# Performance work log

Measured on AMD Instinct MI355X. Metric: run time of the kernel, lower is better.

The kernel has to match this reference:

```python
import math
import jax, jax.numpy as jnp
import numpy as np

S = 2048
HIDDEN = 5120
H = 16              # num_local_heads (128 global heads / TP=8)
NOPE, ROPE, V = 128, 64, 128
QK = NOPE + ROPE    # 192 (module pads to 256; zero-pad is a mathematical no-op)
QLORA, KVLORA = 1536, 512
EPS = 1e-6
BASE, FACTOR = 10000.0, 40.0
BETA_FAST, BETA_SLOW = 32.0, 1.0
ORIG_MAX = 4096
MSCALE = MSCALE_ALL = 0.707


def _yarn_get_mscale(scale, mscale):
    if scale <= 1:
        return 1.0
    return 0.1 * mscale * math.log(scale) + 1.0


SCALING = QK ** -0.5 * _yarn_get_mscale(FACTOR, MSCALE_ALL) ** 2
COS_SIN_MSCALE = _yarn_get_mscale(FACTOR, MSCALE) / _yarn_get_mscale(FACTOR, MSCALE_ALL)


def _yarn_inv_freq():
    half = ROPE // 2
    i = np.arange(half, dtype=np.float64)
    pos_freqs = BASE ** (2.0 * i / ROPE)
    inv_extra = 1.0 / pos_freqs
    inv_interp = 1.0 / (FACTOR * pos_freqs)

    def corr_dim(n_rot):
        return ROPE * math.log(ORIG_MAX / (n_rot * 2 * math.pi)) / (2 * math.log(BASE))

    low = max(math.floor(corr_dim(BETA_FAST)), 0)
    high = min(math.ceil(corr_dim(BETA_SLOW)), ROPE - 1)
    ramp = np.clip((i - low) / max(high - low, 1e-3), 0.0, 1.0)
    inv_freq_mask = 1.0 - ramp  # 1 -> extrapolation, 0 -> interpolation
    inv_freq = inv_interp * (1.0 - inv_freq_mask) + inv_extra * inv_freq_mask
    return jnp.asarray(inv_freq, dtype=jnp.float32)


INV_FREQ = _yarn_inv_freq()  # [ROPE/2]


def _apply_rope(x, cos, sin):
    # non-neox (interleaved pairs): x [S, heads, ROPE], cos/sin [S, ROPE/2]
    x1 = x[..., 0::2]
    x2 = x[..., 1::2]
    c = cos[:, None, :]
    s = sin[:, None, :]
    o1 = x1 * c - x2 * s
    o2 = x2 * c + x1 * s
    return jnp.stack([o1, o2], axis=-1).reshape(x.shape)


def _rms_norm(x, w):
    var = jnp.mean(x.astype(jnp.float32) ** 2, axis=-1, keepdims=True)
    return (x.astype(jnp.float32) * jax.lax.rsqrt(var + EPS)).astype(x.dtype) * w


def setup_inputs() -> dict:
    key = jax.random.key(0)
    ks = jax.random.split(key, 8)
    sd = 0.02
    return {
        'positions': jnp.arange(S, dtype=jnp.int64 if jax.config.jax_enable_x64 else jnp.int32),
        'hidden_states': jax.random.normal(ks[0], (S, HIDDEN), jnp.float32),
        'w_q_a': jax.random.normal(ks[1], (HIDDEN, QLORA), jnp.float32) * sd,
        'q_a_ln_w': jnp.ones((QLORA,), jnp.float32),
        'w_q_b': jax.random.normal(ks[2], (QLORA, H * QK), jnp.float32) * sd,
        'w_kv_a': jax.random.normal(ks[3], (HIDDEN, KVLORA + ROPE), jnp.float32) * sd,
        'kv_a_ln_w': jnp.ones((KVLORA,), jnp.float32),
        'w_kv_b': jax.random.normal(ks[4], (KVLORA, H * (NOPE + V)), jnp.float32) * sd,
        'w_o': jax.random.normal(ks[5], (H * V, HIDDEN), jnp.float32) * sd,
    }


def reference(positions, hidden_states, w_q_a, q_a_ln_w, w_q_b, w_kv_a, kv_a_ln_w, w_kv_b, w_o):
    # Q low-rank path: q_a_proj -> RMSNorm -> q_b_proj
    q = hidden_states @ w_q_a                       # [S, QLORA]
    q = _rms_norm(q, q_a_ln_w)
    q = (q @ w_q_b).reshape(S, H, QK)               # [S, H, 192]
    q_nope, q_pe = q[..., :NOPE], q[..., NOPE:]

    # KV latent path: shared MQA latent + decoupled rope key
    latent = hidden_states @ w_kv_a                 # [S, KVLORA+ROPE]
    kv_a = _rms_norm(latent[:, :KVLORA], kv_a_ln_w)
    k_pe = latent[:, None, KVLORA:]                 # [S, 1, ROPE]
    kv = (kv_a @ w_kv_b).reshape(S, H, NOPE + V)
    k_nope, v = kv[..., :NOPE], kv[..., NOPE:]

    # partial (decoupled) yarn RoPE on the 64-dim rope slice
    freqs = positions.astype(jnp.float32)[:, None] * INV_FREQ[None, :]
    cos = jnp.cos(freqs) * COS_SIN_MSCALE
    sin = jnp.sin(freqs) * COS_SIN_MSCALE
    q_pe = _apply_rope(q_pe, cos, sin)
    k_pe = _apply_rope(k_pe, cos, sin)

    qf = jnp.concatenate([q_nope, q_pe], axis=-1)   # [S, H, 192]
    kf = jnp.concatenate([k_nope, jnp.broadcast_to(k_pe, (S, H, ROPE))], axis=-1)

    # causal paged-attention prefill; zero-padding head dims to 256 is a no-op
    scores = jnp.einsum('qhd,khd->hqk', qf, kf) * SCALING  # [H, S, S]
    causal = jnp.tril(jnp.ones((S, S), dtype=bool))
    scores = jnp.where(causal[None], scores, -jnp.inf)
    probs = jax.nn.softmax(scores, axis=-1)
    attn = jnp.einsum('hqk,khd->qhd', probs, v).reshape(S, H * V)
    return attn @ w_o                               # [S, HIDDEN]
```

## Files before the change

kernel.cpp:

```cpp
#include <hip/hip_runtime.h>
#include <math.h>

typedef unsigned short u16;
typedef unsigned int u32;
typedef __attribute__((ext_vector_type(4))) float f32x4;
typedef __attribute__((ext_vector_type(8))) unsigned short u16x8;
typedef __attribute__((ext_vector_type(4))) unsigned short u16x4;
typedef __attribute__((ext_vector_type(8))) __bf16 bf16x8;

#define DEV __device__ __forceinline__

constexpr int S = 2048;
constexpr int HIDDEN = 5120;
constexpr int H = 16;
constexpr int NOPE = 128, ROPE_D = 64, VD = 128;
constexpr int QKD = NOPE + ROPE_D;
constexpr int QLORA = 1536, KVLORA = 512;
constexpr int KVA_N = KVLORA + ROPE_D;
constexpr float SCALING = 0.11472134f;

DEV u16 f2b(float f) {
  u32 u = __builtin_bit_cast(u32, f);
  u32 r = u + 0x7FFFu + ((u >> 16) & 1u);
  return (u16)(r >> 16);
}
DEV float b2f(u16 h) { return __builtin_bit_cast(float, (u32)h << 16); }

DEV void store_out(float* p, float v) { *p = v; }
DEV void store_out(u16* p, float v) { *p = f2b(v); }

DEV void gload_lds16(const u16* g, u16* l) {
  auto* gp = (const __attribute__((address_space(1))) u16*)g;
  auto* lp = (__attribute__((address_space(3))) u16*)l;
  __builtin_amdgcn_global_load_lds(gp, lp, 16, 0, 0);
}

#define SWZ(row, col) ((col) ^ (((row) & 7) << 3))

DEV void transpose_tile(const float* __restrict__ in, u16* __restrict__ out,
                        int R, int C, int c0, int r0, int tid, float (*tl)[33]) {
  int tx = tid & 31, ty = tid >> 5;
  for (int r = ty; r < 32; r += 8)
    tl[r][tx] = in[(size_t)(r0 + r) * C + c0 + tx];
  __syncthreads();
  for (int r = ty; r < 32; r += 8)
    out[(size_t)(c0 + r) * R + r0 + tx] = f2b(tl[tx][r]);
}

__global__ __launch_bounds__(256) void k_prep(const float* __restrict__ hidden, u16* __restrict__ hs_bf,
                                              const float* __restrict__ w_q_a, u16* __restrict__ bt_qa,
                                              const float* __restrict__ w_kv_a, u16* __restrict__ bt_kva,
                                              const float* __restrict__ w_q_b, u16* __restrict__ bt_qb,
                                              const float* __restrict__ w_kv_b, u16* __restrict__ bt_kvb,
                                              float* __restrict__ cs, float* __restrict__ sn) {
  __shared__ float tl[32][33];
  int b = blockIdx.x, tid = threadIdx.x;
  if (b < 10240) {
    int i = (b * 256 + tid) * 4;
    f32x4 v = *reinterpret_cast<const f32x4*>(hidden + i);
    u16x4 o;
    o[0] = f2b(v[0]); o[1] = f2b(v[1]); o[2] = f2b(v[2]); o[3] = f2b(v[3]);
    *reinterpret_cast<u16x4*>(hs_bf + i) = o;
    return;
  }
  b -= 10240;
  if (b < 7680) {
    transpose_tile(w_q_a, bt_qa, HIDDEN, QLORA, (b % 48) * 32, (b / 48) * 32, tid, tl);
    return;
  }
  b -= 7680;
  if (b < 2880) {
    transpose_tile(w_kv_a, bt_kva, HIDDEN, KVA_N, (b % 18) * 32, (b / 18) * 32, tid, tl);
    return;
  }
  b -= 2880;
  if (b < 4608) {
    transpose_tile(w_q_b, bt_qb, QLORA, H * QKD, (b % 96) * 32, (b / 96) * 32, tid, tl);
    return;
  }
  b -= 4608;
  if (b < 2048) {
    transpose_tile(w_kv_b, bt_kvb, KVLORA, H * 256, (b % 128) * 32, (b / 128) * 32, tid, tl);
    return;
  }
  b -= 2048;
  int idx = b * 256 + tid;
  int s = idx >> 5, j = idx & 31;
  double pf = pow(10000.0, (double)j / 32.0);
  double inv_extra = 1.0 / pf;
  double inv_interp = 1.0 / (40.0 * pf);
  double twopi = 6.283185307179586476925286766559;
  double lnb2 = 2.0 * log(10000.0);
  double lowd = floor(64.0 * log(4096.0 / (32.0 * twopi)) / lnb2);
  if (lowd < 0.0) lowd = 0.0;
  double highd = ceil(64.0 * log(4096.0 / twopi) / lnb2);
  if (highd > 63.0) highd = 63.0;
  double denom = highd - lowd;
  if (denom < 0.001) denom = 0.001;
  double ramp = ((double)j - lowd) / denom;
  ramp = ramp < 0.0 ? 0.0 : (ramp > 1.0 ? 1.0 : ramp);
  float invf = (float)(inv_interp * ramp + inv_extra * (1.0 - ramp));
  float fr = (float)s * invf;
  cs[idx] = cosf(fr);
  sn[idx] = sinf(fr);
}

template <typename OutT>
DEV void gemm_body(u16* Al, u16* Bl, const u16* __restrict__ A,
                   const u16* __restrict__ BT, OutT* __restrict__ C,
                   int N, int Kstride, int Klen, int mbase, int nbase) {
  const int tid = threadIdx.x;
  const int lane = tid & 63, wave = tid >> 6;
  const int wr = wave >> 1, wc = wave & 1;
  const int lr = lane & 15, lk = lane >> 4;
  const int srow = wave * 32 + (lane >> 2);
  const int skoff = (((lane & 3) ^ ((lane >> 3) & 3))) * 8;
  const int swlk8 = (lk ^ ((lr >> 1) & 3)) * 8;
  const u16* aptr = A + (size_t)(mbase + srow) * Kstride + skoff;
  const u16* bptr = BT + (size_t)(nbase + srow) * Kstride + skoff;
  u16* alw = Al + wave * (32 * 32);
  u16* blw = Bl + wave * (32 * 32);

  auto STAGE = [&](int b, int kk) {
    gload_lds16(aptr + kk, alw + b * 4096);
    gload_lds16(aptr + (size_t)16 * Kstride + kk, alw + b * 4096 + 16 * 32);
    gload_lds16(bptr + kk, blw + b * 4096);
    gload_lds16(bptr + (size_t)16 * Kstride + kk, blw + b * 4096 + 16 * 32);
  };

  f32x4 acc[4][4];
#pragma unroll
  for (int mf = 0; mf < 4; ++mf)
#pragma unroll
    for (int nf = 0; nf < 4; ++nf) acc[mf][nf] = {0.f, 0.f, 0.f, 0.f};

  const int nt = Klen >> 5;
  STAGE(0, 0);
  STAGE(1, 32);
  for (int t = 0; t < nt; ++t) {
    const int cur = t & 1;
    if (t + 1 < nt)
      asm volatile("s_waitcnt vmcnt(4)" ::: "memory");
    else
      asm volatile("s_waitcnt vmcnt(0)" ::: "memory");
    __builtin_amdgcn_s_barrier();
    const u16* Ac = Al + cur * 4096;
    const u16* Bc = Bl + cur * 4096;
    bf16x8 af[4], bfr[4];
#pragma unroll
    for (int mf = 0; mf < 4; ++mf)
      af[mf] = *reinterpret_cast<const bf16x8*>(Ac + (wr * 64 + mf * 16 + lr) * 32 + swlk8);
#pragma unroll
    for (int nf = 0; nf < 4; ++nf)
      bfr[nf] = *reinterpret_cast<const bf16x8*>(Bc + (wc * 64 + nf * 16 + lr) * 32 + swlk8);
#pragma unroll
    for (int mf = 0; mf < 4; ++mf)
#pragma unroll
      for (int nf = 0; nf < 4; ++nf)
        acc[mf][nf] = __builtin_amdgcn_mfma_f32_16x16x32_bf16(af[mf], bfr[nf], acc[mf][nf], 0, 0, 0);
    __builtin_amdgcn_s_barrier();
    if (t + 2 < nt) STAGE(cur, (t + 2) * 32);
  }

#pragma unroll
  for (int mf = 0; mf < 4; ++mf)
#pragma unroll
    for (int nf = 0; nf < 4; ++nf) {
      int col = nbase + wc * 64 + nf * 16 + lr;
      if (col < N) {
#pragma unroll
        for (int r = 0; r < 4; ++r) {
          int row = mbase + wr * 64 + mf * 16 + lk * 4 + r;
          store_out(&C[(size_t)row * N + col], acc[mf][nf][r]);
        }
      }
    }
}

__global__ __launch_bounds__(256) void k_gemm_out(const u16* __restrict__ A,
                                                  const u16* __restrict__ BT,
                                                  float* __restrict__ C) {
  __shared__ u16 Al[2 * 128 * 32];
  __shared__ u16 Bl[2 * 128 * 32];
  int id = blockIdx.x;
  int row = id & 15, col = id >> 4;
  gemm_body(Al, Bl, A, BT, C, HIDDEN, H * VD, H * VD, row * 128, col * 128);
}

__global__ __launch_bounds__(256) void k_gemm_up(const u16* __restrict__ Aq, const u16* __restrict__ Bq,
                                                 u16* __restrict__ Cq,
                                                 const u16* __restrict__ Akv, const u16* __restrict__ Bkv,
                                                 u16* __restrict__ Ckv) {
  __shared__ u16 Al[2 * 128 * 32];
  __shared__ u16 Bl[2 * 128 * 32];
  int id = blockIdx.x;
  int row = id & 15, col = id >> 4;
  if (col < 24)
    gemm_body(Al, Bl, Aq, Bq, Cq, H * QKD, QLORA, QLORA, row * 128, col * 128);
  else
    gemm_body(Al, Bl, Akv, Bkv, Ckv, H * 256, KVLORA, KVLORA, row * 128, (col - 24) * 128);
}

__global__ __launch_bounds__(256) void k_gemm_dp(const u16* __restrict__ A,
                                                 const u16* __restrict__ Bq,
                                                 const u16* __restrict__ Bkv,
                                                 float* __restrict__ q0, float* __restrict__ q1,
                                                 float* __restrict__ l0, float* __restrict__ l1) {
  __shared__ u16 Al[2 * 128 * 32];
  __shared__ u16 Bl[2 * 128 * 32];
  constexpr int KH = HIDDEN / 2;
  int id = blockIdx.x;
  int split = id >= 272;
  int u = id - split * 272;
  int row = u & 15, colt = u >> 4;
  const u16* As = A + split * KH;
  if (colt < 12) {
    gemm_body(Al, Bl, As, Bq + split * KH, split ? q1 : q0, QLORA, HIDDEN, KH,
              row * 128, colt * 128);
  } else {
    gemm_body(Al, Bl, As, Bkv + split * KH, split ? l1 : l0, KVA_N, HIDDEN, KH,
              row * 128, (colt - 12) * 128);
  }
}

DEV void rmsnorm2_row(const float* __restrict__ x0, const float* __restrict__ x1,
                      const float* __restrict__ w, u16* __restrict__ y,
                      int ncols, int instride, int row, int tid, float* red) {
  const float* xr0 = x0 + (size_t)row * instride;
  const float* xr1 = x1 + (size_t)row * instride;
  float ss = 0.f;
  for (int i = tid * 4; i < ncols; i += 1024) {
    f32x4 a = *reinterpret_cast<const f32x4*>(xr0 + i);
    f32x4 b = *reinterpret_cast<const f32x4*>(xr1 + i);
    f32x4 v = a + b;
    ss += v[0] * v[0] + v[1] * v[1] + v[2] * v[2] + v[3] * v[3];
  }
  for (int off = 32; off > 0; off >>= 1) ss += __shfl_down(ss, off);
  if ((tid & 63) == 0) red[tid >> 6] = ss;
  __syncthreads();
  ss = red[0] + red[1] + red[2] + red[3];
  float sc = rsqrtf(ss / (float)ncols + 1e-6f);
  u16* yr = y + (size_t)row * ncols;
  for (int i = tid * 4; i < ncols; i += 1024) {
    f32x4 a = *reinterpret_cast<const f32x4*>(xr0 + i);
    f32x4 b = *reinterpret_cast<const f32x4*>(xr1 + i);
    f32x4 v = a + b;
    u16x4 o;
    o[0] = f2b(v[0] * sc * w[i]);
    o[1] = f2b(v[1] * sc * w[i + 1]);
    o[2] = f2b(v[2] * sc * w[i + 2]);
    o[3] = f2b(v[3] * sc * w[i + 3]);
    *reinterpret_cast<u16x4*>(yr + i) = o;
  }
}

__global__ __launch_bounds__(256) void k_mid(const float* __restrict__ q0, const float* __restrict__ q1,
                                             const float* __restrict__ qw, u16* __restrict__ q_ln,
                                             const float* __restrict__ l0, const float* __restrict__ l1,
                                             const float* __restrict__ kw, u16* __restrict__ kv_ln,
                                             const float* __restrict__ w_o, u16* __restrict__ bt_o) {
  __shared__ float red[4];
  __shared__ float tl[32][33];
  int b = blockIdx.x, tid = threadIdx.x;
  if (b < 2048) {
    rmsnorm2_row(q0, q1, qw, q_ln, QLORA, QLORA, b, tid, red);
    return;
  }
  if (b < 4096) {
    rmsnorm2_row(l0, l1, kw, kv_ln, KVLORA, KVA_N, b - 2048, tid, red);
    return;
  }
  int u = b - 4096;
  transpose_tile(w_o, bt_o, H * VD, HIDDEN, (u % 160) * 32, (u / 160) * 32, tid, tl);
}

__global__ __launch_bounds__(256) void k_build(const u16* __restrict__ qn,
                                               const u16* __restrict__ kv,
                                               const float* __restrict__ lat0,
                                               const float* __restrict__ lat1,
                                               const float* __restrict__ cs,
                                               const float* __restrict__ sn,
                                               u16* __restrict__ qf, u16* __restrict__ kf,
                                               u16* __restrict__ vt) {
  __shared__ u16 tv[32][33];
  int b = blockIdx.x, tid = threadIdx.x;
  if (b < 2048) {
    int s = b;
    for (int idx = tid; idx < H * NOPE; idx += 256) {
      int h = idx >> 7, dd = idx & 127;
      qf[((size_t)h * S + s) * QKD + dd] = qn[(size_t)s * (H * QKD) + h * QKD + dd];
      kf[((size_t)h * S + s) * QKD + dd] = kv[(size_t)s * (H * 256) + h * 256 + dd];
    }
    for (int idx = tid; idx < H * 32; idx += 256) {
      int h = idx >> 5, j = idx & 31;
      float c = cs[s * 32 + j], si = sn[s * 32 + j];
      float x1 = b2f(qn[(size_t)s * (H * QKD) + h * QKD + NOPE + 2 * j]);
      float x2 = b2f(qn[(size_t)s * (H * QKD) + h * QKD + NOPE + 2 * j + 1]);
      qf[((size_t)h * S + s) * QKD + NOPE + 2 * j] = f2b(x1 * c - x2 * si);
      qf[((size_t)h * S + s) * QKD + NOPE + 2 * j + 1] = f2b(x2 * c + x1 * si);
      float k1 = lat0[(size_t)s * KVA_N + KVLORA + 2 * j] + lat1[(size_t)s * KVA_N + KVLORA + 2 * j];
      float k2 = lat0[(size_t)s * KVA_N + KVLORA + 2 * j + 1] + lat1[(size_t)s * KVA_N + KVLORA + 2 * j + 1];
      kf[((size_t)h * S + s) * QKD + NOPE + 2 * j] = f2b(k1 * c - k2 * si);
      kf[((size_t)h * S + s) * QKD + NOPE + 2 * j + 1] = f2b(k2 * c + k1 * si);
    }
    return;
  }
  int bb = b - 2048;
  int s0 = (bb & 63) * 32, d0 = ((bb >> 6) & 3) * 32, h = bb >> 8;
  int tx = tid & 31, ty = tid >> 5;
  for (int r = ty; r < 32; r += 8)
    tv[r][tx] = kv[(size_t)(s0 + r) * (H * 256) + h * 256 + NOPE + d0 + tx];
  __syncthreads();
  for (int r = ty; r < 32; r += 8)
    vt[((size_t)h * VD + d0 + r) * S + s0 + tx] = tv[tx][r];
}

__global__ __launch_bounds__(256) void k_attn(const u16* __restrict__ qf,
                                              const u16* __restrict__ kf,
                                              const u16* __restrict__ vt,
                                              u16* __restrict__ attn) {
  const int bidx = blockIdx.x;
  const int j = bidx & 31;
  const int h = bidx >> 5;
  const int qt = (h < 8) ? j : 31 - j;
  const int qbase = qt * 64;
  const int tid = threadIdx.x, wave = tid >> 6, lane = tid & 63;
  const int lr = lane & 15, lk = lane >> 4;
  __shared__ u16 Kl[64][192];
  __shared__ u16 Vl[128][64];
  __shared__ u16 Pl[4][16][64];

  int krow_[6], kofs_[6], vrow_[4], vofs_[4];
#pragma unroll
  for (int i = 0; i < 6; ++i) { int c = tid + i * 256; krow_[i] = c / 24; kofs_[i] = (c % 24) * 8; }
#pragma unroll
  for (int i = 0; i < 4; ++i) { int c = tid + i * 256; vrow_[i] = c >> 3; vofs_[i] = (c & 7) * 8; }
  const u16* kfh = kf + (size_t)h * S * QKD;
  const u16* vth = vt + (size_t)h * VD * S;

  bf16x8 qfrag[6];
  const u16* qrow = qf + ((size_t)h * S + qbase + wave * 16 + lr) * QKD;
#pragma unroll
  for (int d = 0; d < 6; ++d)
    qfrag[d] = *reinterpret_cast<const bf16x8*>(qrow + d * 32 + lk * 8);

  u16x8 kreg[6], vreg[4];
#pragma unroll
  for (int i = 0; i < 6; ++i)
    kreg[i] = *reinterpret_cast<const u16x8*>(kfh + (size_t)krow_[i] * QKD + kofs_[i]);
#pragma unroll
  for (int i = 0; i < 4; ++i)
    vreg[i] = *reinterpret_cast<const u16x8*>(vth + (size_t)vrow_[i] * S + vofs_[i]);

  f32x4 o[8];
#pragma unroll
  for (int f = 0; f < 8; ++f) o[f] = {0.f, 0.f, 0.f, 0.f};
  float m_[4] = {-__builtin_inff(), -__builtin_inff(), -__builtin_inff(), -__builtin_inff()};
  float l_[4] = {0.f, 0.f, 0.f, 0.f};

  const int ktiles = qt + 1;
  for (int kt = 0; kt < ktiles; ++kt) {
    const int kbase = kt * 64;
    __builtin_amdgcn_s_barrier();
#pragma unroll
    for (int i = 0; i < 6; ++i)
      *reinterpret_cast<u16x8*>(&Kl[krow_[i]][SWZ(krow_[i], kofs_[i])]) = kreg[i];
#pragma unroll
    for (int i = 0; i < 4; ++i)
      *reinterpret_cast<u16x8*>(&Vl[vrow_[i]][SWZ(vrow_[i], vofs_[i])]) = vreg[i];
    if (kt + 1 < ktiles) {
      const int nb = kbase + 64;
#pragma unroll
      for (int i = 0; i < 6; ++i)
        kreg[i] = *reinterpret_cast<const u16x8*>(kfh + (size_t)(nb + krow_[i]) * QKD + kofs_[i]);
#pragma unroll
      for (int i = 0; i < 4; ++i)
        vreg[i] = *reinterpret_cast<const u16x8*>(vth + (size_t)vrow_[i] * S + nb + vofs_[i]);
    }
    asm volatile("s_waitcnt lgkmcnt(0)" ::: "memory");
    __builtin_amdgcn_s_barrier();

    f32x4 sacc[4];
#pragma unroll
    for (int nf = 0; nf < 4; ++nf) sacc[nf] = {0.f, 0.f, 0.f, 0.f};
    __builtin_amdgcn_s_setprio(1);
#pragma unroll
    for (int nf = 0; nf < 4; ++nf)
#pragma unroll
      for (int dk = 0; dk < 6; ++dk) {
        int krow = nf * 16 + lr;
        bf16x8 b = *reinterpret_cast<const bf16x8*>(&Kl[krow][SWZ(krow, dk * 32 + lk * 8)]);
        sacc[nf] = __builtin_amdgcn_mfma_f32_16x16x32_bf16(qfrag[dk], b, sacc[nf], 0, 0, 0);
      }
    __builtin_amdgcn_s_setprio(0);

    float sv[4][4];
    float rowmax[4] = {-__builtin_inff(), -__builtin_inff(), -__builtin_inff(), -__builtin_inff()};
#pragma unroll
    for (int nf = 0; nf < 4; ++nf) {
      int kcol = kbase + nf * 16 + lr;
#pragma unroll
      for (int r = 0; r < 4; ++r) {
        float v = sacc[nf][r] * SCALING;
        int qrow_g = qbase + wave * 16 + lk * 4 + r;
        if (kcol > qrow_g) v = -__builtin_inff();
        sv[nf][r] = v;
        rowmax[r] = fmaxf(rowmax[r], v);
      }
    }
#pragma unroll
    for (int r = 0; r < 4; ++r) {
#pragma unroll
      for (int off = 1; off < 16; off <<= 1)
        rowmax[r] = fmaxf(rowmax[r], __shfl_xor(rowmax[r], off));
    }
    float needm = fmaxf(fmaxf(rowmax[0] - m_[0], rowmax[1] - m_[1]),
                        fmaxf(rowmax[2] - m_[2], rowmax[3] - m_[3]));
    if (!__all(needm <= 8.0f)) {
#pragma unroll
      for (int r = 0; r < 4; ++r) {
        float mn = fmaxf(m_[r], rowmax[r]);
        float alpha = __expf(m_[r] - mn);
        m_[r] = mn;
        l_[r] *= alpha;
#pragma unroll
        for (int f = 0; f < 8; ++f) o[f][r] *= alpha;
      }
    }
    float rowsum[4] = {0.f, 0.f, 0.f, 0.f};
#pragma unroll
    for (int nf = 0; nf < 4; ++nf)
#pragma unroll
      for (int r = 0; r < 4; ++r) {
        float p = __expf(sv[nf][r] - m_[r]);
        sv[nf][r] = p;
        rowsum[r] += p;
      }
#pragma unroll
    for (int r = 0; r < 4; ++r) {
#pragma unroll
      for (int off = 1; off < 16; off <<= 1) rowsum[r] += __shfl_xor(rowsum[r], off);
      l_[r] += rowsum[r];
    }
#pragma unroll
    for (int nf = 0; nf < 4; ++nf)
#pragma unroll
      for (int r = 0; r < 4; ++r) {
        int prow = lk * 4 + r;
        Pl[wave][prow][SWZ(prow, nf * 16 + lr)] = f2b(sv[nf][r]);
      }

    __builtin_amdgcn_s_setprio(1);
#pragma unroll
    for (int kk = 0; kk < 2; ++kk) {
      bf16x8 pa = *reinterpret_cast<const bf16x8*>(&Pl[wave][lr][SWZ(lr, kk * 32 + lk * 8)]);
#pragma unroll
      for (int f = 0; f < 8; ++f) {
        int vrow = f * 16 + lr;
        bf16x8 b = *reinterpret_cast<const bf16x8*>(&Vl[vrow][SWZ(vrow, kk * 32 + lk * 8)]);
        o[f] = __builtin_amdgcn_mfma_f32_16x16x32_bf16(pa, b, o[f], 0, 0, 0);
      }
    }
    __builtin_amdgcn_s_setprio(0);
  }

#pragma unroll
  for (int f = 0; f < 8; ++f)
#pragma unroll
    for (int r = 0; r < 4; ++r) {
      int row = qbase + wave * 16 + lk * 4 + r;
      float val = o[f][r] / l_[r];
      attn[(size_t)row * (H * VD) + h * VD + f * 16 + lr] = f2b(val);
    }
}

extern "C" void kernel_launch(void* const* d_in, const int* in_sizes, int n_in,
                              void* d_out, int out_size, void* d_ws, size_t ws_size,
                              hipStream_t stream) {
  (void)in_sizes; (void)n_in; (void)out_size; (void)ws_size;
  const float* hidden    = (const float*)d_in[1];
  const float* w_q_a     = (const float*)d_in[2];
  const float* q_a_ln_w  = (const float*)d_in[3];
  const float* w_q_b     = (const float*)d_in[4];
  const float* w_kv_a    = (const float*)d_in[5];
  const float* kv_a_ln_w = (const float*)d_in[6];
  const float* w_kv_b    = (const float*)d_in[7];
  const float* w_o       = (const float*)d_in[8];
  float* out = (float*)d_out;

  char* ws = (char*)d_ws;
  size_t off = 0;
  auto alloc = [&](size_t bytes) {
    size_t o = off;
    off += (bytes + 255) & ~(size_t)255;
    return o;
  };
  constexpr int KVA_PAD = 640;
  size_t o_hs    = alloc((size_t)S * HIDDEN * 2);
  size_t o_btqa  = alloc((size_t)QLORA * HIDDEN * 2);
  size_t o_btkva = alloc((size_t)KVA_PAD * HIDDEN * 2);
  size_t o_btqb  = alloc((size_t)(H * QKD) * QLORA * 2);
  size_t o_btkvb = alloc((size_t)(H * 256) * KVLORA * 2);
  size_t o_qlat0 = alloc((size_t)S * QLORA * 4);
  size_t o_qlat1 = alloc((size_t)S * QLORA * 4);
  size_t o_lat0  = alloc((size_t)S * KVA_N * 4);
  size_t o_lat1  = alloc((size_t)S * KVA_N * 4);
  size_t o_qln   = alloc((size_t)S * QLORA * 2);
  size_t o_kvln  = alloc((size_t)S * KVLORA * 2);
  size_t o_qn    = alloc((size_t)S * (H * QKD) * 2);
  size_t o_kv    = alloc((size_t)S * (H * 256) * 2);
  size_t o_kf    = alloc((size_t)H * S * QKD * 2);
  size_t o_vt    = alloc((size_t)H * VD * S * 2);
  size_t o_cs    = alloc((size_t)S * 32 * 4);
  size_t o_sn    = alloc((size_t)S * 32 * 4);

  u16* hs_bf  = (u16*)(ws + o_hs);
  u16* bt_qa  = (u16*)(ws + o_btqa);
  u16* bt_kva = (u16*)(ws + o_btkva);
  u16* bt_qb  = (u16*)(ws + o_btqb);
  u16* bt_kvb = (u16*)(ws + o_btkvb);
  float* q_lat0 = (float*)(ws + o_qlat0);
  float* q_lat1 = (float*)(ws + o_qlat1);
  float* lat0   = (float*)(ws + o_lat0);
  float* lat1   = (float*)(ws + o_lat1);
  u16* q_ln  = (u16*)(ws + o_qln);
  u16* kv_ln = (u16*)(ws + o_kvln);
  u16* qn    = (u16*)(ws + o_qn);
  u16* kvb   = (u16*)(ws + o_kv);
  u16* kf    = (u16*)(ws + o_kf);
  u16* vt    = (u16*)(ws + o_vt);
  float* cs = (float*)(ws + o_cs);
  float* sn = (float*)(ws + o_sn);
  u16* qf   = (u16*)(ws + o_hs);
  u16* bt_o = (u16*)(ws + o_btqa);
  u16* attn = (u16*)(ws + o_qlat0);

  k_prep<<<dim3(27712), dim3(256), 0, stream>>>(hidden, hs_bf, w_q_a, bt_qa,
                                                w_kv_a, bt_kva, w_q_b, bt_qb,
                                                w_kv_b, bt_kvb, cs, sn);

  k_gemm_dp<<<dim3(544), dim3(256), 0, stream>>>(hs_bf, bt_qa, bt_kva,
                                                 q_lat0, q_lat1, lat0, lat1);

  k_mid<<<dim3(14336), dim3(256), 0, stream>>>(q_lat0, q_lat1, q_a_ln_w, q_ln,
                                               lat0, lat1, kv_a_ln_w, kv_ln,
                                               w_o, bt_o);

  k_gemm_up<<<dim3(896), dim3(256), 0, stream>>>(q_ln, bt_qb, qn, kv_ln, bt_kvb, kvb);

  k_build<<<dim3(6144), dim3(256), 0, stream>>>(qn, kvb, lat0, lat1, cs, sn, qf, kf, vt);

  k_attn<<<dim3(512), dim3(256), 0, stream>>>(qf, kf, vt, attn);

  k_gemm_out<<<dim3(640), dim3(256), 0, stream>>>(attn, bt_o, out);
}
```

Before: 331.6 us.

## Fuse RoPE and head-major scatter into up-projection GEMM epilogue, drop LDS staging in attention

New measurement: 523.3 us. 1.58x slower.

```diff
diff --git a/kernel.cpp b/kernel.cpp
--- a/kernel.cpp
+++ b/kernel.cpp
@@ -105,10 +105,9 @@
   sn[idx] = sinf(fr);
 }
 
-template <typename OutT>
-DEV void gemm_body(u16* Al, u16* Bl, const u16* __restrict__ A,
-                   const u16* __restrict__ BT, OutT* __restrict__ C,
-                   int N, int Kstride, int Klen, int mbase, int nbase) {
+DEV void gemm_core(u16* Al, u16* Bl, const u16* __restrict__ A,
+                   const u16* __restrict__ BT,
+                   int Kstride, int Klen, int mbase, int nbase, f32x4 (*acc)[4]) {
   const int tid = threadIdx.x;
   const int lane = tid & 63, wave = tid >> 6;
   const int wr = wave >> 1, wc = wave & 1;
@@ -128,7 +127,6 @@
     gload_lds16(bptr + (size_t)16 * Kstride + kk, blw + b * 4096 + 16 * 32);
   };
 
-  f32x4 acc[4][4];
 #pragma unroll
   for (int mf = 0; mf < 4; ++mf)
 #pragma unroll
@@ -161,7 +159,13 @@
     __builtin_amdgcn_s_barrier();
     if (t + 2 < nt) STAGE(cur, (t + 2) * 32);
   }
-
+}
+
+template <typename OutT>
+DEV void gemm_epilogue(f32x4 (*acc)[4], OutT* __restrict__ C, int N, int mbase, int nbase) {
+  const int lane = threadIdx.x & 63, wave = threadIdx.x >> 6;
+  const int wr = wave >> 1, wc = wave & 1;
+  const int lr = lane & 15, lk = lane >> 4;
 #pragma unroll
   for (int mf = 0; mf < 4; ++mf)
 #pragma unroll
@@ -184,21 +188,88 @@
   __shared__ u16 Bl[2 * 128 * 32];
   int id = blockIdx.x;
   int row = id & 15, col = id >> 4;
-  gemm_body(Al, Bl, A, BT, C, HIDDEN, H * VD, H * VD, row * 128, col * 128);
+  f32x4 acc[4][4];
+  gemm_core(Al, Bl, A, BT, H * VD, H * VD, row * 128, col * 128, acc);
+  gemm_epilogue(acc, C, HIDDEN, row * 128, col * 128);
 }
 
 __global__ __launch_bounds__(256) void k_gemm_up(const u16* __restrict__ Aq, const u16* __restrict__ Bq,
-                                                 u16* __restrict__ Cq,
                                                  const u16* __restrict__ Akv, const u16* __restrict__ Bkv,
-                                                 u16* __restrict__ Ckv) {
+                                                 const float* __restrict__ cs, const float* __restrict__ sn,
+                                                 u16* __restrict__ qf, u16* __restrict__ kf,
+                                                 u16* __restrict__ vt) {
   __shared__ u16 Al[2 * 128 * 32];
   __shared__ u16 Bl[2 * 128 * 32];
   int id = blockIdx.x;
-  int row = id & 15, col = id >> 4;
-  if (col < 24)
-    gemm_body(Al, Bl, Aq, Bq, Cq, H * QKD, QLORA, QLORA, row * 128, col * 128);
-  else
-    gemm_body(Al, Bl, Akv, Bkv, Ckv, H * 256, KVLORA, KVLORA, row * 128, (col - 24) * 128);
+  int rowb = id & 15, col = id >> 4;
+  const int mbase = rowb * 128;
+  const int lane = threadIdx.x & 63, wave = threadIdx.x >> 6;
+  const int wr = wave >> 1, wc = wave & 1;
+  const int lr = lane & 15, lk = lane >> 4;
+  f32x4 acc[4][4];
+  if (col < 24) {
+    const int nbase = col * 128;
+    gemm_core(Al, Bl, Aq, Bq, QLORA, QLORA, mbase, nbase, acc);
+#pragma unroll
+    for (int nf = 0; nf < 4; ++nf) {
+      int colb = nbase + wc * 64 + nf * 16;
+      int h = colb / 192;
+      int db = colb - h * 192;
+      size_t qoff = (size_t)h * S * QKD;
+      if (db < NOPE) {
+#pragma unroll
+        for (int mf = 0; mf < 4; ++mf)
+#pragma unroll
+          for (int r = 0; r < 4; ++r) {
+            int row = mbase + wr * 64 + mf * 16 + lk * 4 + r;
+            qf[qoff + (size_t)row * QKD + db + lr] = f2b(acc[mf][nf][r]);
+          }
+      } else {
+        int jj = (db - NOPE + lr) >> 1;
+        bool odd = lr & 1;
+#pragma unroll
+        for (int mf = 0; mf < 4; ++mf)
+#pragma unroll
+          for (int r = 0; r < 4; ++r) {
+            int row = mbase + wr * 64 + mf * 16 + lk * 4 + r;
+            float val = acc[mf][nf][r];
+            float part = __shfl_xor(val, 1);
+            float c = cs[row * 32 + jj], s = sn[row * 32 + jj];
+            float o = odd ? (val * c + part * s) : (val * c - part * s);
+            qf[qoff + (size_t)row * QKD + db + lr] = f2b(o);
+          }
+      }
+    }
+  } else {
+    const int nbase = (col - 24) * 128;
+    gemm_core(Al, Bl, Akv, Bkv, KVLORA, KVLORA, mbase, nbase, acc);
+#pragma unroll
+    for (int nf = 0; nf < 4; ++nf) {
+      int colb = nbase + wc * 64 + nf * 16;
+      int h = colb >> 8;
+      int db = colb & 255;
+      if (db < NOPE) {
+        size_t koff = (size_t)h * S * QKD;
+#pragma unroll
+        for (int mf = 0; mf < 4; ++mf)
+#pragma unroll
+          for (int r = 0; r < 4; ++r) {
+            int row = mbase + wr * 64 + mf * 16 + lk * 4 + r;
+            kf[koff + (size_t)row * QKD + db + lr] = f2b(acc[mf][nf][r]);
+          }
+      } else {
+        int vtrow = h * VD + db - NOPE + lr;
+#pragma unroll
+        for (int mf = 0; mf < 4; ++mf) {
+          int row0 = mbase + wr * 64 + mf * 16 + lk * 4;
+          u16x4 pk;
+          pk[0] = f2b(acc[mf][nf][0]); pk[1] = f2b(acc[mf][nf][1]);
+          pk[2] = f2b(acc[mf][nf][2]); pk[3] = f2b(acc[mf][nf][3]);
+          *reinterpret_cast<u16x4*>(&vt[(size_t)vtrow * S + row0]) = pk;
+        }
+      }
+    }
+  }
 }
 
 __global__ __launch_bounds__(256) void k_gemm_dp(const u16* __restrict__ A,
@@ -214,12 +285,13 @@
   int u = id - split * 272;
   int row = u & 15, colt = u >> 4;
   const u16* As = A + split * KH;
+  f32x4 acc[4][4];
   if (colt < 12) {
-    gemm_body(Al, Bl, As, Bq + split * KH, split ? q1 : q0, QLORA, HIDDEN, KH,
-              row * 128, colt * 128);
+    gemm_core(Al, Bl, As, Bq + split * KH, HIDDEN, KH, row * 128, colt * 128, acc);
+    gemm_epilogue(acc, split ? q1 : q0, QLORA, row * 128, colt * 128);
   } else {
-    gemm_body(Al, Bl, As, Bkv + split * KH, split ? l1 : l0, KVA_N, HIDDEN, KH,
-              row * 128, (colt - 12) * 128);
+    gemm_core(Al, Bl, As, Bkv + split * KH, HIDDEN, KH, row * 128, (colt - 12) * 128, acc);
+    gemm_epilogue(acc, split ? l1 : l0, KVA_N, row * 128, (colt - 12) * 128);
   }
 }
 
@@ -258,7 +330,9 @@
                                              const float* __restrict__ qw, u16* __restrict__ q_ln,
                                              const float* __restrict__ l0, const float* __restrict__ l1,
                                              const float* __restrict__ kw, u16* __restrict__ kv_ln,
-                                             const float* __restrict__ w_o, u16* __restrict__ bt_o) {
+                                             const float* __restrict__ w_o, u16* __restrict__ bt_o,
+                                             const float* __restrict__ cs, const float* __restrict__ sn,
+                                             u16* __restrict__ kf) {
   __shared__ float red[4];
   __shared__ float tl[32][33];
   int b = blockIdx.x, tid = threadIdx.x;
@@ -270,71 +344,35 @@
     rmsnorm2_row(l0, l1, kw, kv_ln, KVLORA, KVA_N, b - 2048, tid, red);
     return;
   }
-  int u = b - 4096;
-  transpose_tile(w_o, bt_o, H * VD, HIDDEN, (u % 160) * 32, (u / 160) * 32, tid, tl);
-}
-
-__global__ __launch_bounds__(256) void k_build(const u16* __restrict__ qn,
-                                               const u16* __restrict__ kv,
-                                               const float* __restrict__ lat0,
-                                               const float* __restrict__ lat1,
-                                               const float* __restrict__ cs,
-                                               const float* __restrict__ sn,
-                                               u16* __restrict__ qf, u16* __restrict__ kf,
-                                               u16* __restrict__ vt) {
-  __shared__ u16 tv[32][33];
-  int b = blockIdx.x, tid = threadIdx.x;
-  if (b < 2048) {
-    int s = b;
-    for (int idx = tid; idx < H * NOPE; idx += 256) {
-      int h = idx >> 7, dd = idx & 127;
-      qf[((size_t)h * S + s) * QKD + dd] = qn[(size_t)s * (H * QKD) + h * QKD + dd];
-      kf[((size_t)h * S + s) * QKD + dd] = kv[(size_t)s * (H * 256) + h * 256 + dd];
-    }
-    for (int idx = tid; idx < H * 32; idx += 256) {
-      int h = idx >> 5, j = idx & 31;
-      float c = cs[s * 32 + j], si = sn[s * 32 + j];
-      float x1 = b2f(qn[(size_t)s * (H * QKD) + h * QKD + NOPE + 2 * j]);
-      float x2 = b2f(qn[(size_t)s * (H * QKD) + h * QKD + NOPE + 2 * j + 1]);
-      qf[((size_t)h * S + s) * QKD + NOPE + 2 * j] = f2b(x1 * c - x2 * si);
-      qf[((size_t)h * S + s) * QKD + NOPE + 2 * j + 1] = f2b(x2 * c + x1 * si);
-      float k1 = lat0[(size_t)s * KVA_N + KVLORA + 2 * j] + lat1[(size_t)s * KVA_N + KVLORA + 2 * j];
-      float k2 = lat0[(size_t)s * KVA_N + KVLORA + 2 * j + 1] + lat1[(size_t)s * KVA_N + KVLORA + 2 * j + 1];
-      kf[((size_t)h * S + s) * QKD + NOPE + 2 * j] = f2b(k1 * c - k2 * si);
-      kf[((size_t)h * S + s) * QKD + NOPE + 2 * j + 1] = f2b(k2 * c + k1 * si);
-    }
-    return;
-  }
-  int bb = b - 2048;
-  int s0 = (bb & 63) * 32, d0 = ((bb >> 6) & 3) * 32, h = bb >> 8;
-  int tx = tid & 31, ty = tid >> 5;
-  for (int r = ty; r < 32; r += 8)
-    tv[r][tx] = kv[(size_t)(s0 + r) * (H * 256) + h * 256 + NOPE + d0 + tx];
-  __syncthreads();
-  for (int r = ty; r < 32; r += 8)
-    vt[((size_t)h * VD + d0 + r) * S + s0 + tx] = tv[tx][r];
+  if (b < 14336) {
+    int u = b - 4096;
+    transpose_tile(w_o, bt_o, H * VD, HIDDEN, (u % 160) * 32, (u / 160) * 32, tid, tl);
+    return;
+  }
+  int s = b - 14336;
+  for (int idx = tid; idx < H * 32; idx += 256) {
+    int h = idx >> 5, j = idx & 31;
+    float c = cs[s * 32 + j], si = sn[s * 32 + j];
+    float k1 = l0[(size_t)s * KVA_N + KVLORA + 2 * j] + l1[(size_t)s * KVA_N + KVLORA + 2 * j];
+    float k2 = l0[(size_t)s * KVA_N + KVLORA + 2 * j + 1] + l1[(size_t)s * KVA_N + KVLORA + 2 * j + 1];
+    kf[((size_t)h * S + s) * QKD + NOPE + 2 * j] = f2b(k1 * c - k2 * si);
+    kf[((size_t)h * S + s) * QKD + NOPE + 2 * j + 1] = f2b(k2 * c + k1 * si);
+  }
 }
 
 __global__ __launch_bounds__(256) void k_attn(const u16* __restrict__ qf,
                                               const u16* __restrict__ kf,
                                               const u16* __restrict__ vt,
                                               u16* __restrict__ attn) {
-  const int bidx = blockIdx.x;
-  const int j = bidx & 31;
-  const int h = bidx >> 5;
-  const int qt = (h < 8) ? j : 31 - j;
+  const int bid = blockIdx.x;
+  const int h = bid & 15;
+  const int j = bid >> 4;
+  const int qt = (j < 16) ? j : 47 - j;
   const int qbase = qt * 64;
   const int tid = threadIdx.x, wave = tid >> 6, lane = tid & 63;
   const int lr = lane & 15, lk = lane >> 4;
-  __shared__ u16 Kl[64][192];
-  __shared__ u16 Vl[128][64];
   __shared__ u16 Pl[4][16][64];
 
-  int krow_[6], kofs_[6], vrow_[4], vofs_[4];
-#pragma unroll
-  for (int i = 0; i < 6; ++i) { int c = tid + i * 256; krow_[i] = c / 24; kofs_[i] = (c % 24) * 8; }
-#pragma unroll
-  for (int i = 0; i < 4; ++i) { int c = tid + i * 256; vrow_[i] = c >> 3; vofs_[i] = (c & 7) * 8; }
   const u16* kfh = kf + (size_t)h * S * QKD;
   const u16* vth = vt + (size_t)h * VD * S;
 
@@ -343,14 +381,6 @@
 #pragma unroll
   for (int d = 0; d < 6; ++d)
     qfrag[d] = *reinterpret_cast<const bf16x8*>(qrow + d * 32 + lk * 8);
-
-  u16x8 kreg[6], vreg[4];
-#pragma unroll
-  for (int i = 0; i < 6; ++i)
-    kreg[i] = *reinterpret_cast<const u16x8*>(kfh + (size_t)krow_[i] * QKD + kofs_[i]);
-#pragma unroll
-  for (int i = 0; i < 4; ++i)
-    vreg[i] = *reinterpret_cast<const u16x8*>(vth + (size_t)vrow_[i] * S + vofs_[i]);
 
   f32x4 o[8];
 #pragma unroll
@@ -361,37 +391,20 @@
   const int ktiles = qt + 1;
   for (int kt = 0; kt < ktiles; ++kt) {
     const int kbase = kt * 64;
-    __builtin_amdgcn_s_barrier();
-#pragma unroll
-    for (int i = 0; i < 6; ++i)
-      *reinterpret_cast<u16x8*>(&Kl[krow_[i]][SWZ(krow_[i], kofs_[i])]) = kreg[i];
-#pragma unroll
-    for (int i = 0; i < 4; ++i)
-      *reinterpret_cast<u16x8*>(&Vl[vrow_[i]][SWZ(vrow_[i], vofs_[i])]) = vreg[i];
-    if (kt + 1 < ktiles) {
-      const int nb = kbase + 64;
-#pragma unroll
-      for (int i = 0; i < 6; ++i)
-        kreg[i] = *reinterpret_cast<const u16x8*>(kfh + (size_t)(nb + krow_[i]) * QKD + kofs_[i]);
-#pragma unroll
-      for (int i = 0; i < 4; ++i)
-        vreg[i] = *reinterpret_cast<const u16x8*>(vth + (size_t)vrow_[i] * S + nb + vofs_[i]);
-    }
-    asm volatile("s_waitcnt lgkmcnt(0)" ::: "memory");
-    __builtin_amdgcn_s_barrier();
 
     f32x4 sacc[4];
 #pragma unroll
     for (int nf = 0; nf < 4; ++nf) sacc[nf] = {0.f, 0.f, 0.f, 0.f};
     __builtin_amdgcn_s_setprio(1);
 #pragma unroll
-    for (int nf = 0; nf < 4; ++nf)
+    for (int nf = 0; nf < 4; ++nf) {
+      const u16* kp = kfh + (size_t)(kbase + nf * 16 + lr) * QKD + lk * 8;
 #pragma unroll
       for (int dk = 0; dk < 6; ++dk) {
-        int krow = nf * 16 + lr;
-        bf16x8 b = *reinterpret_cast<const bf16x8*>(&Kl[krow][SWZ(krow, dk * 32 + lk * 8)]);
+        bf16x8 b = *reinterpret_cast<const bf16x8*>(kp + dk * 32);
         sacc[nf] = __builtin_amdgcn_mfma_f32_16x16x32_bf16(qfrag[dk], b, sacc[nf], 0, 0, 0);
       }
+    }
     __builtin_amdgcn_s_setprio(0);
 
     float sv[4][4];
@@ -456,8 +469,8 @@
       bf16x8 pa = *reinterpret_cast<const bf16x8*>(&Pl[wave][lr][SWZ(lr, kk * 32 + lk * 8)]);
 #pragma unroll
       for (int f = 0; f < 8; ++f) {
-        int vrow = f * 16 + lr;
-        bf16x8 b = *reinterpret_cast<const bf16x8*>(&Vl[vrow][SWZ(vrow, kk * 32 + lk * 8)]);
+        const u16* vp = vth + (size_t)(f * 16 + lr) * S + kbase + kk * 32 + lk * 8;
+        bf16x8 b = *reinterpret_cast<const bf16x8*>(vp);
         o[f] = __builtin_amdgcn_mfma_f32_16x16x32_bf16(pa, b, o[f], 0, 0, 0);
       }
     }
@@ -507,8 +520,6 @@
   size_t o_lat1  = alloc((size_t)S * KVA_N * 4);
   size_t o_qln   = alloc((size_t)S * QLORA * 2);
   size_t o_kvln  = alloc((size_t)S * KVLORA * 2);
-  size_t o_qn    = alloc((size_t)S * (H * QKD) * 2);
-  size_t o_kv    = alloc((size_t)S * (H * 256) * 2);
   size_t o_kf    = alloc((size_t)H * S * QKD * 2);
   size_t o_vt    = alloc((size_t)H * VD * S * 2);
   size_t o_cs    = alloc((size_t)S * 32 * 4);
@@ -525,8 +536,6 @@
   float* lat1   = (float*)(ws + o_lat1);
   u16* q_ln  = (u16*)(ws + o_qln);
   u16* kv_ln = (u16*)(ws + o_kvln);
-  u16* qn    = (u16*)(ws + o_qn);
-  u16* kvb   = (u16*)(ws + o_kv);
   u16* kf    = (u16*)(ws + o_kf);
   u16* vt    = (u16*)(ws + o_vt);
   float* cs = (float*)(ws + o_cs);
@@ -542,13 +551,12 @@
   k_gemm_dp<<<dim3(544), dim3(256), 0, stream>>>(hs_bf, bt_qa, bt_kva,
                                                  q_lat0, q_lat1, lat0, lat1);
 
-  k_mid<<<dim3(14336), dim3(256), 0, stream>>>(q_lat0, q_lat1, q_a_ln_w, q_ln,
+  k_mid<<<dim3(16384), dim3(256), 0, stream>>>(q_lat0, q_lat1, q_a_ln_w, q_ln,
                                                lat0, lat1, kv_a_ln_w, kv_ln,
-                                               w_o, bt_o);
-
-  k_gemm_up<<<dim3(896), dim3(256), 0, stream>>>(q_ln, bt_qb, qn, kv_ln, bt_kvb, kvb);
-
-  k_build<<<dim3(6144), dim3(256), 0, stream>>>(qn, kvb, lat0, lat1, cs, sn, qf, kf, vt);
+                                               w_o, bt_o, cs, sn, kf);
+
+  k_gemm_up<<<dim3(896), dim3(256), 0, stream>>>(q_ln, bt_qb, kv_ln, bt_kvb,
+                                                 cs, sn, qf, kf, vt);
 
   k_attn<<<dim3(512), dim3(256), 0, stream>>>(qf, kf, vt, attn);
 
```
